# Kernel tuning notes

Measured on AMD Instinct MI355X. Metric: run time of the kernel, lower is better.

The kernel has to match this reference:

```python
import jax, jax.numpy as jnp
import numpy as np

L, H = 6, 8          # n_layer, n_head
LN_EPS = 1e-5


def _ln(x, g, b):
    mu = jnp.mean(x, axis=-1, keepdims=True)
    var = jnp.mean((x - mu) ** 2, axis=-1, keepdims=True)
    return (x - mu) * jax.lax.rsqrt(var + LN_EPS) * g + b


def setup_inputs() -> dict:
    key = jax.random.key(0)
    B, T, V, D = 2, 2048, 32000, 512
    F = 4 * D
    std = 0.02
    ks = jax.random.split(key, 8)
    idx = jax.random.randint(ks[0], (B, T), 0, V)
    wte = jax.random.normal(ks[1], (V, D), dtype=jnp.float32) * std
    wpe = jax.random.normal(ks[2], (T, D), dtype=jnp.float32) * std
    qkv_w = jax.random.normal(ks[3], (L, D, 3 * D), dtype=jnp.float32) * std
    proj_w = jax.random.normal(ks[4], (L, D, D), dtype=jnp.float32) * std
    fc1_w = jax.random.normal(ks[5], (L, D, F), dtype=jnp.float32) * std
    fc2_w = jax.random.normal(ks[6], (L, F, D), dtype=jnp.float32) * std
    return dict(
        idx=idx, wte=wte, wpe=wpe,
        ln1_g=jnp.ones((L, D), jnp.float32), ln1_b=jnp.zeros((L, D), jnp.float32),
        qkv_w=qkv_w, qkv_b=jnp.zeros((L, 3 * D), jnp.float32),
        proj_w=proj_w, proj_b=jnp.zeros((L, D), jnp.float32),
        ln2_g=jnp.ones((L, D), jnp.float32), ln2_b=jnp.zeros((L, D), jnp.float32),
        fc1_w=fc1_w, fc1_b=jnp.zeros((L, F), jnp.float32),
        fc2_w=fc2_w, fc2_b=jnp.zeros((L, D), jnp.float32),
        lnf_g=jnp.ones((D,), jnp.float32), lnf_b=jnp.zeros((D,), jnp.float32),
    )


def reference(idx, wte, wpe, ln1_g, ln1_b, qkv_w, qkv_b, proj_w, proj_b,
              ln2_g, ln2_b, fc1_w, fc1_b, fc2_w, fc2_b, lnf_g, lnf_b):
    B, T = idx.shape
    D = wte.shape[1]
    hd = D // H
    scale = 1.0 / jnp.sqrt(jnp.asarray(hd, wte.dtype))
    x = wte[idx] + wpe[:T]                      # [B,T,D]
    mask = jnp.tril(jnp.ones((T, T), dtype=bool))

    def block(x, p):
        g1, b1, Wqkv, bqkv, Wp, bp, g2, b2, W1, bf1, W2, bf2 = p
        h = _ln(x, g1, b1)
        qkv = h @ Wqkv + bqkv                   # [B,T,3D]
        q, k, v = jnp.split(qkv, 3, axis=-1)
        q = q.reshape(B, T, H, hd)
        k = k.reshape(B, T, H, hd)
        v = v.reshape(B, T, H, hd)
        att = jnp.einsum('bqhd,bkhd->bhqk', q, k) * scale
        att = jnp.where(mask, att, -jnp.inf)
        att = jax.nn.softmax(att, axis=-1)
        y = jnp.einsum('bhqk,bkhd->bqhd', att, v).reshape(B, T, D)
        x = x + y @ Wp + bp
        h = _ln(x, g2, b2)
        x = x + jax.nn.gelu(h @ W1 + bf1, approximate=False) @ W2 + bf2
        return x, None

    x, _ = jax.lax.scan(block, x, (ln1_g, ln1_b, qkv_w, qkv_b, proj_w, proj_b,
                                   ln2_g, ln2_b, fc1_w, fc1_b, fc2_w, fc2_b))
    x = _ln(x, lnf_g, lnf_b)
    logits = x @ wte.T                          # tied head, [B,T,V]
    return logits
```

## Files before the change

### kernel.cpp

```cpp
#include <hip/hip_runtime.h>
#include <hip/hip_bf16.h>
#include <math.h>

#define BB 2
#define TT 2048
#define DD 512
#define HH 8
#define HD 64
#define FF 2048
#define VV 32000
#define LL 6
#define MM (BB * TT)

typedef unsigned int   u32;
typedef unsigned short u16;
typedef __attribute__((ext_vector_type(8))) short short8;
typedef __attribute__((ext_vector_type(4))) float f32x4;

__device__ __forceinline__ u16 f2bf_bits(float f)
{
    __hip_bfloat16 h = __float2bfloat16(f);
    u16 u;
    __builtin_memcpy(&u, &h, 2);
    return u;
}

__device__ __forceinline__ void gll16(const u16* g, u16* l)
{
    __builtin_amdgcn_global_load_lds(
        (const __attribute__((address_space(1))) u32*)g,
        (__attribute__((address_space(3))) u32*)l,
        16, 0, 0);
}

__device__ __forceinline__ float gelu_exact(float v)
{
    return 0.5f * v * (1.0f + erff(v * 0.70710678118654752440f));
}

__device__ __forceinline__ u16* swp(u16* base, int row, int col)
{
    int off = (row * 128 + col * 2) ^ ((row & 7) << 4);
    return (u16*)((char*)base + off);
}
__device__ __forceinline__ const u16* swpc(const u16* base, int row, int col)
{
    int off = (row * 128 + col * 2) ^ ((row & 7) << 4);
    return (const u16*)((const char*)base + off);
}

__global__ __launch_bounds__(128)
void embed_kernel(const int* __restrict__ idx, const float* __restrict__ wte,
                  const float* __restrict__ wpe, float* __restrict__ x)
{
    int row = blockIdx.x;
    int t = row & (TT - 1);
    int tok = idx[row];
    const float4* wt = (const float4*)(wte + (size_t)tok * DD);
    const float4* wp = (const float4*)(wpe + (size_t)t * DD);
    float4 a = wt[threadIdx.x];
    float4 p = wp[threadIdx.x];
    float4 r;
    r.x = a.x + p.x; r.y = a.y + p.y; r.z = a.z + p.z; r.w = a.w + p.w;
    ((float4*)(x + (size_t)row * DD))[threadIdx.x] = r;
}

__global__ __launch_bounds__(256)
void ln_kernel(const float* __restrict__ x, const float* __restrict__ g,
               const float* __restrict__ b, u16* __restrict__ out)
{
    int row = blockIdx.x;
    const float* xr = x + (size_t)row * DD;
    int tid = threadIdx.x;
    float v1 = xr[tid], v2 = xr[tid + 256];
    float s = v1 + v2;
    float ss = v1 * v1 + v2 * v2;
    #pragma unroll
    for (int o = 32; o; o >>= 1) {
        s  += __shfl_xor(s, o);
        ss += __shfl_xor(ss, o);
    }
    __shared__ float sred[4], ssred[4];
    int wid = tid >> 6, lane = tid & 63;
    if (lane == 0) { sred[wid] = s; ssred[wid] = ss; }
    __syncthreads();
    s  = sred[0] + sred[1] + sred[2] + sred[3];
    ss = ssred[0] + ssred[1] + ssred[2] + ssred[3];
    float mu  = s * (1.0f / DD);
    float var = ss * (1.0f / DD) - mu * mu;
    float rs  = rsqrtf(var + 1e-5f);
    u16* orow = out + (size_t)row * DD;
    orow[tid]       = f2bf_bits((v1 - mu) * rs * g[tid]       + b[tid]);
    orow[tid + 256] = f2bf_bits((v2 - mu) * rs * g[tid + 256] + b[tid + 256]);
}

__global__ __launch_bounds__(256)
void weight_prep_kernel(const float* __restrict__ qkv_w, const float* __restrict__ proj_w,
                        const float* __restrict__ fc1_w, const float* __restrict__ fc2_w,
                        u16* __restrict__ wqa, u16* __restrict__ wpa,
                        u16* __restrict__ w1a, u16* __restrict__ w2a)
{
    int id = blockIdx.x;
    int l = id / 3072, r = id % 3072;
    const float* in; u16* out; int K, N, tt;
    if (r < 768)       { in = qkv_w + (size_t)l * DD * 3 * DD; out = wqa + (size_t)l * 3 * DD * DD; K = DD; N = 3 * DD; tt = r; }
    else if (r < 1024) { in = proj_w + (size_t)l * DD * DD;    out = wpa + (size_t)l * DD * DD;    K = DD; N = DD;     tt = r - 768; }
    else if (r < 2048) { in = fc1_w + (size_t)l * DD * FF;     out = w1a + (size_t)l * DD * FF;    K = DD; N = FF;     tt = r - 1024; }
    else               { in = fc2_w + (size_t)l * FF * DD;     out = w2a + (size_t)l * FF * DD;    K = FF; N = DD;     tt = r - 2048; }
    int ntx = N >> 5;
    int n0 = (tt % ntx) << 5, k0 = (tt / ntx) << 5;
    __shared__ float tile[32][33];
    int tx = threadIdx.x & 31, ty = threadIdx.x >> 5;
    #pragma unroll
    for (int i = 0; i < 4; ++i)
        tile[ty + i * 8][tx] = in[(size_t)(k0 + ty + i * 8) * N + n0 + tx];
    __syncthreads();
    #pragma unroll
    for (int i = 0; i < 4; ++i)
        out[(size_t)(n0 + ty + i * 8) * K + k0 + tx] = f2bf_bits(tile[tx][ty + i * 8]);
}

__global__ __launch_bounds__(256)
void cvt_kernel(const float* __restrict__ in, u16* __restrict__ out, int n4)
{
    int i = blockIdx.x * 256 + threadIdx.x;
    if (i >= n4) return;
    float4 v = ((const float4*)in)[i];
    ushort4 o;
    o.x = f2bf_bits(v.x); o.y = f2bf_bits(v.y);
    o.z = f2bf_bits(v.z); o.w = f2bf_bits(v.w);
    ((ushort4*)out)[i] = o;
}

template<int BN, bool GELU_ACT, bool RESID, bool OUTBF16, bool QKV_SPLIT>
__global__ __launch_bounds__(256)
void mfma_gemm(const u16* __restrict__ A, const u16* __restrict__ Bt,
               const float* __restrict__ bias, const float* __restrict__ resid,
               void* __restrict__ Cout, u16* __restrict__ Vout,
               int M, int N, int K)
{
    constexpr int NJ = BN / 32;
    __shared__ u16 As[2][128 * 64];
    __shared__ u16 Bs[2][BN * 64];

    const int tid  = threadIdx.x;
    const int lane = tid & 63;
    const int w    = tid >> 6;
    const int wr   = w >> 1, wc = w & 1;

    const int nbx = gridDim.x;
    const int nwg = nbx * gridDim.y;
    int bid = blockIdx.y * nbx + blockIdx.x;
    int swz = (bid & 7) * (nwg >> 3) + (bid >> 3);
    const int m0 = (swz / nbx) * 128;
    const int n0 = (swz % nbx) * BN;

    const int trow = tid >> 3;
    const int tcol = (tid & 7) * 8;
    const u16* ga = A  + (size_t)(m0 + trow) * K + tcol;
    const u16* gb = Bt + (size_t)(n0 + trow) * K + tcol;

    auto stage = [&](int buf, int k0) {
        u16* la = As[buf] + tid * 8;
        u16* lb = Bs[buf] + tid * 8;
        #pragma unroll
        for (int p = 0; p < 4; ++p)
            gll16(ga + k0 + (size_t)p * 32 * K, la + p * 2048);
        #pragma unroll
        for (int p = 0; p < NJ; ++p)
            gll16(gb + k0 + (size_t)p * 32 * K, lb + p * 2048);
    };

    f32x4 acc[4][NJ] = {};

    const int fr = lane & 15;
    const int fk = (lane >> 4) * 8;

    const int nt = K >> 6;
    stage(0, 0);
    for (int t = 0; t < nt; ++t) {
        asm volatile("s_waitcnt vmcnt(0)" ::: "memory");
        __syncthreads();
        if (t + 1 < nt) stage((t + 1) & 1, (t + 1) << 6);

        const u16* as = As[t & 1];
        const u16* bs = Bs[t & 1];
        #pragma unroll
        for (int ks = 0; ks < 2; ++ks) {
            short8 af[4], bfr[NJ];
            #pragma unroll
            for (int f = 0; f < 4; ++f)
                af[f]  = *(const short8*)&as[(wr * 64 + f * 16 + fr) * 64 + ks * 32 + fk];
            #pragma unroll
            for (int f = 0; f < NJ; ++f)
                bfr[f] = *(const short8*)&bs[(wc * (BN / 2) + f * 16 + fr) * 64 + ks * 32 + fk];
            #pragma unroll
            for (int i = 0; i < 4; ++i)
                #pragma unroll
                for (int j = 0; j < NJ; ++j)
                    acc[i][j] = __builtin_amdgcn_mfma_f32_16x16x32_bf16(
                        af[i], bfr[j], acc[i][j], 0, 0, 0);
        }
    }

    const int c0 = n0 + wc * (BN / 2) + fr;
    const int r0 = m0 + wr * 64 + ((lane >> 4) << 2);
    #pragma unroll
    for (int j = 0; j < NJ; ++j) {
        const int c = c0 + j * 16;
        const float bv = bias ? bias[c] : 0.0f;
        #pragma unroll
        for (int i = 0; i < 4; ++i) {
            const int row0 = r0 + i * 16;
            if constexpr (QKV_SPLIT) {
                if (c < 1024) {
                    #pragma unroll
                    for (int r = 0; r < 4; ++r)
                        ((u16*)Cout)[(size_t)(row0 + r) * 1024 + c] =
                            f2bf_bits(acc[i][j][r] + bv);
                } else {
                    ushort4 o;
                    o.x = f2bf_bits(acc[i][j][0] + bv);
                    o.y = f2bf_bits(acc[i][j][1] + bv);
                    o.z = f2bf_bits(acc[i][j][2] + bv);
                    o.w = f2bf_bits(acc[i][j][3] + bv);
                    const int t0 = row0 & (TT - 1);
                    *(ushort4*)&Vout[(((size_t)(row0 >> 11) * 512 + (c - 1024)) << 11) + t0] = o;
                }
            } else {
                #pragma unroll
                for (int r = 0; r < 4; ++r) {
                    const int row = row0 + r;
                    float v = acc[i][j][r] + bv;
                    if constexpr (GELU_ACT) v = gelu_exact(v);
                    if constexpr (RESID) v += resid[(size_t)row * N + c];
                    if constexpr (OUTBF16)
                        ((u16*)Cout)[(size_t)row * N + c] = f2bf_bits(v);
                    else
                        ((float*)Cout)[(size_t)row * N + c] = v;
                }
            }
        }
    }
}

__global__ __launch_bounds__(256)
void attn_kernel(const u16* __restrict__ qkb, const u16* __restrict__ vtb,
                 u16* __restrict__ y)
{
    const int l = blockIdx.x;
    const int u = l & 255, v = l >> 8;
    const int bh = u & 15;
    const int half = u >> 4;
    const int qt = v ? (16 + half) : (15 - half);
    const int h = bh & (HH - 1);
    const int b = bh >> 3;

    __shared__ alignas(16) u16 Qs[4096];
    __shared__ alignas(16) u16 Ks[2][4096];
    __shared__ alignas(16) u16 Vt[2][4096];
    __shared__ alignas(16) u16 Ps[4096];

    const int tid = threadIdx.x;
    const int lane = tid & 63;
    const int w = tid >> 6;
    const int ln = lane & 15, hi = lane >> 4;
    const int q0 = qt * 64;

    const u16* base  = qkb + (size_t)b * TT * 1024 + h * HD;
    const u16* vbase = vtb + (size_t)(b * 512 + h * HD) * TT;

    const int sr = tid >> 2, sc = (tid & 3) * 16;

    {
        const u16* qrow = base + (size_t)(q0 + sr) * 1024;
        *(short8*)swp(Qs, sr, sc)     = *(const short8*)(qrow + sc);
        *(short8*)swp(Qs, sr, sc + 8) = *(const short8*)(qrow + sc + 8);
    }
    short8 rk0, rk1, rv0, rv1;
    {
        const u16* krow = base + (size_t)sr * 1024 + 512;
        rk0 = *(const short8*)(krow + sc);
        rk1 = *(const short8*)(krow + sc + 8);
        const u16* vrow = vbase + (size_t)sr * TT;
        rv0 = *(const short8*)(vrow + sc);
        rv1 = *(const short8*)(vrow + sc + 8);
    }
    __syncthreads();

    short8 aq0 = *(const short8*)swpc(Qs, w * 16 + ln, hi * 8);
    short8 aq1 = *(const short8*)swpc(Qs, w * 16 + ln, 32 + hi * 8);

    const float SC = 0.18033688011112042f;

    float m[4], lsum[4];
    f32x4 oacc[4] = {};
    #pragma unroll
    for (int r = 0; r < 4; ++r) { m[r] = -INFINITY; lsum[r] = 0.0f; }

    for (int kt = 0; kt <= qt; ++kt) {
        u16* ks = Ks[kt & 1];
        u16* vt = Vt[kt & 1];

        *(short8*)swp(ks, sr, sc)     = rk0;
        *(short8*)swp(ks, sr, sc + 8) = rk1;
        *(short8*)swp(vt, sr, sc)     = rv0;
        *(short8*)swp(vt, sr, sc + 8) = rv1;
        __syncthreads();

        if (kt < qt) {
            const int k0n = (kt + 1) * 64;
            const u16* krow = base + (size_t)(k0n + sr) * 1024 + 512;
            rk0 = *(const short8*)(krow + sc);
            rk1 = *(const short8*)(krow + sc + 8);
            const u16* vrow = vbase + (size_t)sr * TT + k0n;
            rv0 = *(const short8*)(vrow + sc);
            rv1 = *(const short8*)(vrow + sc + 8);
        }

        f32x4 sacc[4] = {};
        __builtin_amdgcn_s_setprio(1);
        #pragma unroll
        for (int j = 0; j < 4; ++j) {
            short8 bk0 = *(const short8*)swpc(ks, j * 16 + ln, hi * 8);
            short8 bk1 = *(const short8*)swpc(ks, j * 16 + ln, 32 + hi * 8);
            sacc[j] = __builtin_amdgcn_mfma_f32_16x16x32_bf16(aq0, bk0, sacc[j], 0, 0, 0);
            sacc[j] = __builtin_amdgcn_mfma_f32_16x16x32_bf16(aq1, bk1, sacc[j], 0, 0, 0);
        }
        __builtin_amdgcn_s_setprio(0);

        const bool diag = (kt == qt);
        #pragma unroll
        for (int r = 0; r < 4; ++r) {
            const int qrow = w * 16 + hi * 4 + r;
            float sv[4];
            #pragma unroll
            for (int j = 0; j < 4; ++j) {
                float s = sacc[j][r] * SC;
                if (diag && (j * 16 + ln > qrow)) s = -INFINITY;
                sv[j] = s;
            }
            float rm = fmaxf(fmaxf(sv[0], sv[1]), fmaxf(sv[2], sv[3]));
            #pragma unroll
            for (int o = 1; o < 16; o <<= 1) rm = fmaxf(rm, __shfl_xor(rm, o));
            float mn = fmaxf(m[r], rm);
            float corr = exp2f(m[r] - mn);
            m[r] = mn;
            float p0 = exp2f(sv[0] - mn);
            float p1 = exp2f(sv[1] - mn);
            float p2 = exp2f(sv[2] - mn);
            float p3 = exp2f(sv[3] - mn);
            *swp(Ps, qrow, ln)      = f2bf_bits(p0);
            *swp(Ps, qrow, 16 + ln) = f2bf_bits(p1);
            *swp(Ps, qrow, 32 + ln) = f2bf_bits(p2);
            *swp(Ps, qrow, 48 + ln) = f2bf_bits(p3);
            lsum[r] = lsum[r] * corr + ((p0 + p1) + (p2 + p3));
            #pragma unroll
            for (int db = 0; db < 4; ++db) oacc[db][r] *= corr;
        }

        short8 ap0 = *(const short8*)swpc(Ps, w * 16 + ln, hi * 8);
        short8 ap1 = *(const short8*)swpc(Ps, w * 16 + ln, 32 + hi * 8);
        __builtin_amdgcn_s_setprio(1);
        #pragma unroll
        for (int db = 0; db < 4; ++db) {
            short8 bv0 = *(const short8*)swpc(vt, db * 16 + ln, hi * 8);
            short8 bv1 = *(const short8*)swpc(vt, db * 16 + ln, 32 + hi * 8);
            oacc[db] = __builtin_amdgcn_mfma_f32_16x16x32_bf16(ap0, bv0, oacc[db], 0, 0, 0);
            oacc[db] = __builtin_amdgcn_mfma_f32_16x16x32_bf16(ap1, bv1, oacc[db], 0, 0, 0);
        }
        __builtin_amdgcn_s_setprio(0);
    }

    #pragma unroll
    for (int r = 0; r < 4; ++r) {
        float lt = lsum[r];
        #pragma unroll
        for (int o = 1; o < 16; o <<= 1) lt += __shfl_xor(lt, o);
        const int q = q0 + w * 16 + hi * 4 + r;
        const float inv = 1.0f / lt;
        u16* yrow = y + (size_t)(b * TT + q) * DD + h * HD;
        #pragma unroll
        for (int db = 0; db < 4; ++db)
            yrow[db * 16 + ln] = f2bf_bits(oacc[db][r] * inv);
    }
}

extern "C" void kernel_launch(void* const* d_in, const int* in_sizes, int n_in,
                              void* d_out, int out_size, void* d_ws, size_t ws_size,
                              hipStream_t stream)
{
    const int*   idx    = (const int*)  d_in[0];
    const float* wte    = (const float*)d_in[1];
    const float* wpe    = (const float*)d_in[2];
    const float* ln1_g  = (const float*)d_in[3];
    const float* ln1_b  = (const float*)d_in[4];
    const float* qkv_w  = (const float*)d_in[5];
    const float* qkv_b  = (const float*)d_in[6];
    const float* proj_w = (const float*)d_in[7];
    const float* proj_b = (const float*)d_in[8];
    const float* ln2_g  = (const float*)d_in[9];
    const float* ln2_b  = (const float*)d_in[10];
    const float* fc1_w  = (const float*)d_in[11];
    const float* fc1_b  = (const float*)d_in[12];
    const float* fc2_w  = (const float*)d_in[13];
    const float* fc2_b  = (const float*)d_in[14];
    const float* lnf_g  = (const float*)d_in[15];
    const float* lnf_b  = (const float*)d_in[16];
    float* out = (float*)d_out;

    char* ws = (char*)d_ws;
    float* x    = (float*)(ws);
    u16*   h    = (u16*)(ws + ((size_t)8  << 20));
    u16*   y    = (u16*)(ws + ((size_t)12 << 20));
    u16*   qkb  = (u16*)(ws + ((size_t)16 << 20));
    u16*   vtb  = (u16*)(ws + ((size_t)24 << 20));
    u16*   wqa  = (u16*)(ws + ((size_t)28 << 20));
    u16*   wpa  = (u16*)(ws + ((size_t)38 << 20));
    u16*   w1a  = (u16*)(ws + ((size_t)42 << 20));
    u16*   w2a  = (u16*)(ws + ((size_t)55 << 20));
    u16*   ffb  = (u16*)(ws + ((size_t)68 << 20));
    u16*   wteb = (u16*)(ws + ((size_t)85 << 20));

    embed_kernel<<<MM, 128, 0, stream>>>(idx, wte, wpe, x);

    weight_prep_kernel<<<LL * 3072, 256, 0, stream>>>(
        qkv_w, proj_w, fc1_w, fc2_w, wqa, wpa, w1a, w2a);

    cvt_kernel<<<(VV * DD / 4 + 255) / 256, 256, 0, stream>>>(wte, wteb, VV * DD / 4);

    for (int l = 0; l < LL; ++l) {
        ln_kernel<<<MM, 256, 0, stream>>>(x, ln1_g + l * DD, ln1_b + l * DD, h);

        mfma_gemm<128, false, false, true, true><<<dim3(12, 32), 256, 0, stream>>>(
            h, wqa + (size_t)l * 3 * DD * DD, qkv_b + (size_t)l * 3 * DD,
            nullptr, qkb, vtb, MM, 3 * DD, DD);

        attn_kernel<<<512, 256, 0, stream>>>(qkb, vtb, y);

        mfma_gemm<64, false, true, false, false><<<dim3(8, 32), 256, 0, stream>>>(
            y, wpa + (size_t)l * DD * DD, proj_b + (size_t)l * DD,
            x, x, nullptr, MM, DD, DD);

        ln_kernel<<<MM, 256, 0, stream>>>(x, ln2_g + l * DD, ln2_b + l * DD, h);

        mfma_gemm<128, true, false, true, false><<<dim3(16, 32), 256, 0, stream>>>(
            h, w1a + (size_t)l * DD * FF, fc1_b + (size_t)l * FF,
            nullptr, ffb, nullptr, MM, FF, DD);

        mfma_gemm<64, false, true, false, false><<<dim3(8, 32), 256, 0, stream>>>(
            ffb, w2a + (size_t)l * FF * DD, fc2_b + (size_t)l * DD,
            x, x, nullptr, MM, DD, FF);
    }

    ln_kernel<<<MM, 256, 0, stream>>>(x, lnf_g, lnf_b, h);

    mfma_gemm<128, false, false, false, false><<<dim3(250, 32), 256, 0, stream>>>(
        h, wteb, nullptr, nullptr, out, nullptr, MM, VV, DD);
}
```

Measured before the change: 1.159 ms.

## Add dedicated triple-buffered LM-head GEMM and DPP row-max in attention

Measured after the change: 1.181 ms. No clear change (+1.9%).

```diff
diff --git a/kernel.cpp b/kernel.cpp
--- a/kernel.cpp
+++ b/kernel.cpp
@@ -47,6 +47,15 @@
 {
     int off = (row * 128 + col * 2) ^ ((row & 7) << 4);
     return (const u16*)((const char*)base + off);
+}
+
+template<int CTRL>
+__device__ __forceinline__ float fmax_dpp(float v)
+{
+    union { float f; int i; } a, b;
+    a.f = v;
+    b.i = __builtin_amdgcn_mov_dpp(a.i, CTRL, 0xf, 0xf, true);
+    return fmaxf(v, b.f);
 }
 
 __global__ __launch_bounds__(128)
@@ -244,6 +253,115 @@
     }
 }
 
+__global__ __launch_bounds__(512)
+void head_gemm(const u16* __restrict__ A, const u16* __restrict__ Bt,
+               float* __restrict__ C, int M, int N, int K)
+{
+    __shared__ u16 As3[3][256 * 64];
+    __shared__ u16 Bs3[3][128 * 64];
+
+    const int tid  = threadIdx.x;
+    const int lane = tid & 63;
+    const int w    = tid >> 6;
+    const int wm   = w >> 2, wn = w & 3;
+    const int ln   = lane & 15, hi = lane >> 4;
+
+    const int cpx = gridDim.x >> 3;
+    int bid = blockIdx.x;
+    int swz = (bid & 7) * cpx + (bid >> 3);
+    const int m0 = (swz & 15) * 256;
+    const int n0 = (swz >> 4) * 128;
+
+    const int srow = tid >> 3;
+    const int sch  = tid & 7;
+
+    auto stageA = [&](int b, int t, int p) {
+        int r = p * 64 + srow;
+        int ch = sch ^ (r & 7);
+        gll16(A + (size_t)(m0 + r) * K + t * 64 + ch * 8,
+              As3[b] + (size_t)p * 4096 + (size_t)tid * 8);
+    };
+    auto stageB = [&](int b, int t, int p) {
+        int r = p * 64 + srow;
+        int ch = sch ^ (r & 7);
+        gll16(Bt + (size_t)(n0 + r) * K + t * 64 + ch * 8,
+              Bs3[b] + (size_t)p * 4096 + (size_t)tid * 8);
+    };
+    auto rdA = [&](int b, int i, int ks) -> short8 {
+        int row = wm * 128 + i * 16 + ln;
+        int off = (row << 7) + (((ks << 6) + (hi << 4)) ^ ((row & 7) << 4));
+        return *(const short8*)((const char*)As3[b] + off);
+    };
+    auto rdB = [&](int b, int j, int ks) -> short8 {
+        int row = wn * 32 + j * 16 + ln;
+        int off = (row << 7) + (((ks << 6) + (hi << 4)) ^ ((row & 7) << 4));
+        return *(const short8*)((const char*)Bs3[b] + off);
+    };
+
+    f32x4 acc[8][2] = {};
+    const int nt = K >> 6;
+
+    #pragma unroll
+    for (int p = 0; p < 4; ++p) stageA(0, 0, p);
+    stageB(0, 0, 0); stageB(0, 0, 1);
+    #pragma unroll
+    for (int p = 0; p < 4; ++p) stageA(1, 1, p);
+    stageB(1, 1, 0); stageB(1, 1, 1);
+
+    for (int t = 0; t < nt; ++t) {
+        const int b  = t % 3;
+        const int bn = (t + 2) % 3;
+        const bool st = (t + 2) < nt;
+
+        if (t + 1 < nt)
+            asm volatile("s_waitcnt vmcnt(6)" ::: "memory");
+        else
+            asm volatile("s_waitcnt vmcnt(0)" ::: "memory");
+        asm volatile("s_barrier" ::: "memory");
+        __builtin_amdgcn_sched_barrier(0);
+
+        short8 af[8], bf0, bf1;
+
+        #pragma unroll
+        for (int i = 0; i < 8; ++i) af[i] = rdA(b, i, 0);
+        bf0 = rdB(b, 0, 0); bf1 = rdB(b, 1, 0);
+        if (st) { stageA(bn, t + 2, 0); stageA(bn, t + 2, 1); stageA(bn, t + 2, 2); }
+        asm volatile("s_barrier" ::: "memory");
+        __builtin_amdgcn_sched_barrier(0);
+        __builtin_amdgcn_s_setprio(1);
+        #pragma unroll
+        for (int i = 0; i < 8; ++i) {
+            acc[i][0] = __builtin_amdgcn_mfma_f32_16x16x32_bf16(af[i], bf0, acc[i][0], 0, 0, 0);
+            acc[i][1] = __builtin_amdgcn_mfma_f32_16x16x32_bf16(af[i], bf1, acc[i][1], 0, 0, 0);
+        }
+        __builtin_amdgcn_s_setprio(0);
+
+        #pragma unroll
+        for (int i = 0; i < 8; ++i) af[i] = rdA(b, i, 1);
+        bf0 = rdB(b, 0, 1); bf1 = rdB(b, 1, 1);
+        if (st) { stageA(bn, t + 2, 3); stageB(bn, t + 2, 0); stageB(bn, t + 2, 1); }
+        asm volatile("s_barrier" ::: "memory");
+        __builtin_amdgcn_sched_barrier(0);
+        __builtin_amdgcn_s_setprio(1);
+        #pragma unroll
+        for (int i = 0; i < 8; ++i) {
+            acc[i][0] = __builtin_amdgcn_mfma_f32_16x16x32_bf16(af[i], bf0, acc[i][0], 0, 0, 0);
+            acc[i][1] = __builtin_amdgcn_mfma_f32_16x16x32_bf16(af[i], bf1, acc[i][1], 0, 0, 0);
+        }
+        __builtin_amdgcn_s_setprio(0);
+    }
+
+    const int c0 = n0 + wn * 32 + ln;
+    const int r0 = m0 + wm * 128 + (hi << 2);
+    #pragma unroll
+    for (int i = 0; i < 8; ++i)
+        #pragma unroll
+        for (int j = 0; j < 2; ++j)
+            #pragma unroll
+            for (int r = 0; r < 4; ++r)
+                C[(size_t)(r0 + i * 16 + r) * N + c0 + j * 16] = acc[i][j][r];
+}
+
 __global__ __launch_bounds__(256)
 void attn_kernel(const u16* __restrict__ qkb, const u16* __restrict__ vtb,
                  u16* __restrict__ y)
@@ -335,17 +453,25 @@
             const int qrow = w * 16 + hi * 4 + r;
             float sv[4];
             #pragma unroll
-            for (int j = 0; j < 4; ++j) {
-                float s = sacc[j][r] * SC;
-                if (diag && (j * 16 + ln > qrow)) s = -INFINITY;
-                sv[j] = s;
+            for (int j = 0; j < 4; ++j) sv[j] = sacc[j][r] * SC;
+            if (diag) {
+                #pragma unroll
+                for (int j = 0; j < 4; ++j)
+                    if (j * 16 + ln > qrow) sv[j] = -INFINITY;
             }
             float rm = fmaxf(fmaxf(sv[0], sv[1]), fmaxf(sv[2], sv[3]));
-            #pragma unroll
-            for (int o = 1; o < 16; o <<= 1) rm = fmaxf(rm, __shfl_xor(rm, o));
-            float mn = fmaxf(m[r], rm);
-            float corr = exp2f(m[r] - mn);
-            m[r] = mn;
+            rm = fmax_dpp<0x121>(rm);
+            rm = fmax_dpp<0x122>(rm);
+            rm = fmax_dpp<0x124>(rm);
+            rm = fmax_dpp<0x128>(rm);
+            if (rm > m[r]) {
+                float corr = exp2f(m[r] - rm);
+                m[r] = rm;
+                lsum[r] *= corr;
+                #pragma unroll
+                for (int db = 0; db < 4; ++db) oacc[db][r] *= corr;
+            }
+            const float mn = m[r];
             float p0 = exp2f(sv[0] - mn);
             float p1 = exp2f(sv[1] - mn);
             float p2 = exp2f(sv[2] - mn);
@@ -354,9 +480,7 @@
             *swp(Ps, qrow, 16 + ln) = f2bf_bits(p1);
             *swp(Ps, qrow, 32 + ln) = f2bf_bits(p2);
             *swp(Ps, qrow, 48 + ln) = f2bf_bits(p3);
-            lsum[r] = lsum[r] * corr + ((p0 + p1) + (p2 + p3));
-            #pragma unroll
-            for (int db = 0; db < 4; ++db) oacc[db][r] *= corr;
+            lsum[r] += (p0 + p1) + (p2 + p3);
         }
 
         short8 ap0 = *(const short8*)swpc(Ps, w * 16 + ln, hi * 8);
@@ -455,6 +579,5 @@
 
     ln_kernel<<<MM, 256, 0, stream>>>(x, lnf_g, lnf_b, h);
 
-    mfma_gemm<128, false, false, false, false><<<dim3(250, 32), 256, 0, stream>>>(
-        h, wteb, nullptr, nullptr, out, nullptr, MM, VV, DD);
-}
+    head_gemm<<<4000, 512, 0, stream>>>(h, wteb, out, MM, VV, DD);
+}
```

## Permute V and P key order, use DPP row max, skip softmax rescale

Applied to the files above, without the earlier changes.

Result: slower. 1.201 ms (+3.6%).

```diff
diff --git a/kernel.cpp b/kernel.cpp
--- a/kernel.cpp
+++ b/kernel.cpp
@@ -47,6 +47,15 @@
 {
     int off = (row * 128 + col * 2) ^ ((row & 7) << 4);
     return (const u16*)((const char*)base + off);
+}
+
+template<int CTRL>
+__device__ __forceinline__ float fmax_dpp(float v)
+{
+    union { float f; int i; } a, b;
+    a.f = v;
+    b.i = __builtin_amdgcn_mov_dpp(a.i, CTRL, 0xf, 0xf, true);
+    return fmaxf(v, b.f);
 }
 
 __global__ __launch_bounds__(128)
@@ -219,13 +228,13 @@
                         ((u16*)Cout)[(size_t)(row0 + r) * 1024 + c] =
                             f2bf_bits(acc[i][j][r] + bv);
                 } else {
-                    ushort4 o;
-                    o.x = f2bf_bits(acc[i][j][0] + bv);
-                    o.y = f2bf_bits(acc[i][j][1] + bv);
-                    o.z = f2bf_bits(acc[i][j][2] + bv);
-                    o.w = f2bf_bits(acc[i][j][3] + bv);
                     const int t0 = row0 & (TT - 1);
-                    *(ushort4*)&Vout[(((size_t)(row0 >> 11) * 512 + (c - 1024)) << 11) + t0] = o;
+                    const size_t vrow = ((size_t)(row0 >> 11) * 512 + (c - 1024)) << 11;
+                    const int pb = (t0 & ~63) | (((t0 & 15) << 2) | ((t0 >> 4) & 3));
+                    Vout[vrow + pb]      = f2bf_bits(acc[i][j][0] + bv);
+                    Vout[vrow + pb + 4]  = f2bf_bits(acc[i][j][1] + bv);
+                    Vout[vrow + pb + 8]  = f2bf_bits(acc[i][j][2] + bv);
+                    Vout[vrow + pb + 12] = f2bf_bits(acc[i][j][3] + bv);
                 }
             } else {
                 #pragma unroll
@@ -335,28 +344,35 @@
             const int qrow = w * 16 + hi * 4 + r;
             float sv[4];
             #pragma unroll
-            for (int j = 0; j < 4; ++j) {
-                float s = sacc[j][r] * SC;
-                if (diag && (j * 16 + ln > qrow)) s = -INFINITY;
-                sv[j] = s;
+            for (int j = 0; j < 4; ++j) sv[j] = sacc[j][r] * SC;
+            if (diag) {
+                #pragma unroll
+                for (int j = 0; j < 4; ++j)
+                    if (j * 16 + ln > qrow) sv[j] = -INFINITY;
             }
             float rm = fmaxf(fmaxf(sv[0], sv[1]), fmaxf(sv[2], sv[3]));
-            #pragma unroll
-            for (int o = 1; o < 16; o <<= 1) rm = fmaxf(rm, __shfl_xor(rm, o));
-            float mn = fmaxf(m[r], rm);
-            float corr = exp2f(m[r] - mn);
-            m[r] = mn;
+            rm = fmax_dpp<0x121>(rm);
+            rm = fmax_dpp<0x122>(rm);
+            rm = fmax_dpp<0x124>(rm);
+            rm = fmax_dpp<0x128>(rm);
+            if (rm > m[r]) {
+                float corr = exp2f(m[r] - rm);
+                m[r] = rm;
+                lsum[r] *= corr;
+                #pragma unroll
+                for (int db = 0; db < 4; ++db) oacc[db][r] *= corr;
+            }
+            const float mn = m[r];
             float p0 = exp2f(sv[0] - mn);
             float p1 = exp2f(sv[1] - mn);
             float p2 = exp2f(sv[2] - mn);
             float p3 = exp2f(sv[3] - mn);
-            *swp(Ps, qrow, ln)      = f2bf_bits(p0);
-            *swp(Ps, qrow, 16 + ln) = f2bf_bits(p1);
-            *swp(Ps, qrow, 32 + ln) = f2bf_bits(p2);
-            *swp(Ps, qrow, 48 + ln) = f2bf_bits(p3);
-            lsum[r] = lsum[r] * corr + ((p0 + p1) + (p2 + p3));
-            #pragma unroll
-            for (int db = 0; db < 4; ++db) oacc[db][r] *= corr;
+            u32 pk0 = (u32)f2bf_bits(p0) | ((u32)f2bf_bits(p1) << 16);
+            u32 pk1 = (u32)f2bf_bits(p2) | ((u32)f2bf_bits(p3) << 16);
+            char* pdst = (char*)Ps + (((qrow << 7) + (ln << 3)) ^ ((qrow & 7) << 4));
+            uint2 pv; pv.x = pk0; pv.y = pk1;
+            *(uint2*)pdst = pv;
+            lsum[r] += (p0 + p1) + (p2 + p3);
         }
 
         short8 ap0 = *(const short8*)swpc(Ps, w * 16 + ln, hi * 8);
```
